# Optimization experiments

Hardware: AMD Instinct MI355X
Metric: run time of the kernel (lower is better)

The kernel has to match this reference:

```python
import jax, jax.numpy as jnp
import numpy as np

B, H, O, E, CMAP = 8192, 1024, 256, 16, 1000


def setup_inputs() -> dict:
    key = jax.random.key(0)
    k_x, k_w, k_b, k_num, k_c = jax.random.split(key, 5)
    x = jax.random.normal(k_x, (B, H), dtype=jnp.float32)
    num = jax.random.randint(k_num, (B,), 0, CMAP, dtype=jnp.int64)
    c = jax.random.randint(k_c, (CMAP,), 0, E, dtype=jnp.int64)
    # per-expert Linear params (torch default: uniform(-1/sqrt(H), 1/sqrt(H)))
    bound = 1.0 / np.sqrt(H)
    W = jax.random.uniform(k_w, (E, O, H), dtype=jnp.float32, minval=-bound, maxval=bound)
    b = jax.random.uniform(k_b, (E, O), dtype=jnp.float32, minval=-bound, maxval=bound)
    return {"x": x, "W": W, "b": b, "num": num, "c": c}


def reference(x, W, b, num, c):
    # expert id for each sample: layers[c[num[i]]]
    expert = c[num]  # [B]
    # compute all experts' linear outputs in one batched GEMM, then select.
    # logits: [B, E, O]
    logits = jnp.einsum('bh,eoh->beo', x, W) + b[None, :, :]
    sel = jnp.take_along_axis(logits, expert[:, None, None], axis=1)[:, 0, :]  # [B, O]
    return jax.nn.sigmoid(sel)
```

## Files before the change

kernel.cpp:

```cpp
#include <hip/hip_runtime.h>
#include <hip/hip_bf16.h>
#include <stdint.h>

#define B_N   8192
#define H_K   1024
#define O_N   256
#define E_N   16
#define RCAP  1024

#define TILE_M    64
#define TILE_N    128
#define BK        64
#define NITER     (H_K / BK)
#define MAX_TILES (RCAP / TILE_M)

#define WS_CURSOR   0
#define WS_ROWBUF   1024
#define WS_XSORT    131072
#define WS_WBF16    (WS_XSORT + 33554432 + 131072)

typedef __attribute__((ext_vector_type(8))) short  short8;
typedef __attribute__((ext_vector_type(4))) float  float4v;

__device__ __forceinline__ short f32_to_bf16(float f) {
    uint32_t u = __builtin_bit_cast(uint32_t, f);
    u += 0x7fffu + ((u >> 16) & 1u);
    return (short)(u >> 16);
}

__device__ __forceinline__ short8 cvt8(float4v v0, float4v v1) {
    short8 s;
    s[0] = f32_to_bf16(v0[0]); s[1] = f32_to_bf16(v0[1]);
    s[2] = f32_to_bf16(v0[2]); s[3] = f32_to_bf16(v0[3]);
    s[4] = f32_to_bf16(v1[0]); s[5] = f32_to_bf16(v1[1]);
    s[6] = f32_to_bf16(v1[2]); s[7] = f32_to_bf16(v1[3]);
    return s;
}

__device__ __forceinline__ float4v mfma16(short8 a, short8 b, float4v c) {
    return __builtin_amdgcn_mfma_f32_16x16x32_bf16(a, b, c, 0, 0, 0);
}

__device__ __forceinline__ void gl2lds16(const void* gsrc, void* ldst) {
    __builtin_amdgcn_global_load_lds(
        (const __attribute__((address_space(1))) uint32_t*)gsrc,
        (__attribute__((address_space(3))) uint32_t*)ldst, 16, 0, 0);
}

__global__ __launch_bounds__(256) void
k_prep(const float* __restrict__ W, const int* __restrict__ num, const int* __restrict__ c,
       int* __restrict__ cursor, int* __restrict__ rowbuf, short* __restrict__ Wb) {
    const int tid = threadIdx.x;
    const int bx  = blockIdx.x;

    if (bx < 32) {
        __shared__ int lcnt[E_N], lbase[E_N], lcnt2[E_N];
        if (tid < E_N) { lcnt[tid] = 0; lcnt2[tid] = 0; }
        __syncthreads();
        const int i = bx * 256 + tid;
        const int e = c[num[i]];
        atomicAdd(&lcnt[e], 1);
        __syncthreads();
        if (tid < E_N) lbase[tid] = atomicAdd(&cursor[tid], lcnt[tid]);
        __syncthreads();
        const int r = atomicAdd(&lcnt2[e], 1);
        const int p = lbase[e] + r;
        if (p < RCAP) rowbuf[e * RCAP + p] = i;
    }

    const int nchunk = E_N * O_N * H_K / 8;
    const int stride = gridDim.x * blockDim.x;
    for (int ch = bx * 256 + tid; ch < nchunk; ch += stride) {
        const float4v* src = (const float4v*)(W + (size_t)ch * 8);
        *(short8*)(Wb + (size_t)ch * 8) = cvt8(src[0], src[1]);
    }
}

__global__ __launch_bounds__(256) void
k_reorder(const float* __restrict__ x, const int* __restrict__ cursor,
          const int* __restrict__ rowbuf, short* __restrict__ xsrt) {
    const int e = blockIdx.x, t = blockIdx.y, tid = threadIdx.x;
    int count = cursor[e]; if (count > RCAP) count = RCAP;
    const int lim = (count + TILE_M - 1) & ~(TILE_M - 1);
    const int p0 = t * 32;
    if (p0 >= lim) return;

#pragma unroll
    for (int it = 0; it < 16; ++it) {
        const int idx = tid + it * 256;
        const int rl = idx >> 7, ch = idx & 127;
        const int p = p0 + rl;
        if (p >= lim) continue;
        short8 s;
        if (p < count) {
            const int grow = rowbuf[e * RCAP + p];
            const float4v* src = (const float4v*)(x + (size_t)grow * H_K + ch * 8);
            s = cvt8(src[0], src[1]);
        } else {
            s = (short8)(short)0;
        }
        *(short8*)(xsrt + ((size_t)(e * RCAP + p)) * H_K + ch * 8) = s;
    }
}

__global__ __launch_bounds__(256) void
k_gemm(const short* __restrict__ xs_g, const short* __restrict__ Wb,
       const float* __restrict__ bias, const int* __restrict__ cursor,
       const int* __restrict__ rowbuf, float* __restrict__ out) {
    const int e = blockIdx.x;
    int count = cursor[e]; if (count > RCAP) count = RCAP;
    const int m0 = blockIdx.y * TILE_M;
    if (m0 >= count) return;
    const int n0 = blockIdx.z * TILE_N;

    __shared__ short xs[2][TILE_M][BK];
    __shared__ short wsh[2][TILE_N][BK];
    __shared__ int   rows[TILE_M];

    const int tid = threadIdx.x;
    if (tid < TILE_M)
        rows[tid] = (m0 + tid < count) ? rowbuf[e * RCAP + m0 + tid] : -1;

    const int lane = tid & 63;
    const int wave = tid >> 6;
    const int wm = wave >> 1, wn = wave & 1;
    const int quad = lane >> 4, l16 = lane & 15;

    const int sub = lane >> 3;
    const int clx = (lane & 7) ^ sub;

    const short* xseg = xs_g + (size_t)(e * RCAP + m0) * H_K;
    const short* wseg = Wb + (size_t)(e * O_N + n0) * H_K;

    auto issue = [&](int buf, int k0) {
#pragma unroll
        for (int u = 0; u < 2; ++u) {
            const int q = wave * 2 + u;
            gl2lds16(xseg + (size_t)(q * 8 + sub) * H_K + k0 + clx * 8, &xs[buf][q * 8][0]);
        }
#pragma unroll
        for (int u = 0; u < 4; ++u) {
            const int q = wave * 4 + u;
            gl2lds16(wseg + (size_t)(q * 8 + sub) * H_K + k0 + clx * 8, &wsh[buf][q * 8][0]);
        }
    };

    float4v acc[2][4];
#pragma unroll
    for (int i = 0; i < 2; ++i)
#pragma unroll
        for (int j = 0; j < 4; ++j) acc[i][j] = (float4v)0.0f;

    issue(0, 0);

    for (int k = 0; k < NITER; ++k) {
        const int cur = k & 1;
        __syncthreads();
        if (k + 1 < NITER) issue(1 - cur, (k + 1) * BK);

#pragma unroll
        for (int ks = 0; ks < 2; ++ks) {
            const int cl = ks * 4 + quad;
            const int cp = (cl ^ (l16 & 7)) * 8;
            short8 a0 = *(const short8*)&xs[cur][wm * 32 + l16][cp];
            short8 a1 = *(const short8*)&xs[cur][wm * 32 + 16 + l16][cp];
            short8 b0 = *(const short8*)&wsh[cur][wn * 64 + l16][cp];
            short8 b1 = *(const short8*)&wsh[cur][wn * 64 + 16 + l16][cp];
            short8 b2 = *(const short8*)&wsh[cur][wn * 64 + 32 + l16][cp];
            short8 b3 = *(const short8*)&wsh[cur][wn * 64 + 48 + l16][cp];
            acc[0][0] = mfma16(a0, b0, acc[0][0]);
            acc[0][1] = mfma16(a0, b1, acc[0][1]);
            acc[0][2] = mfma16(a0, b2, acc[0][2]);
            acc[0][3] = mfma16(a0, b3, acc[0][3]);
            acc[1][0] = mfma16(a1, b0, acc[1][0]);
            acc[1][1] = mfma16(a1, b1, acc[1][1]);
            acc[1][2] = mfma16(a1, b2, acc[1][2]);
            acc[1][3] = mfma16(a1, b3, acc[1][3]);
        }
    }

#pragma unroll
    for (int jn = 0; jn < 4; ++jn) {
        const int colg = n0 + wn * 64 + jn * 16 + l16;
        const float bv = bias[e * O_N + colg];
#pragma unroll
        for (int jm = 0; jm < 2; ++jm) {
            const int rl = wm * 32 + jm * 16 + quad * 4;
#pragma unroll
            for (int reg = 0; reg < 4; ++reg) {
                const int rid = rows[rl + reg];
                if (rid >= 0) {
                    const float v = acc[jm][jn][reg] + bv;
                    out[(size_t)rid * O_N + colg] = 1.0f / (1.0f + __expf(-v));
                }
            }
        }
    }
}

extern "C" void kernel_launch(void* const* d_in, const int* in_sizes, int n_in,
                              void* d_out, int out_size, void* d_ws, size_t ws_size,
                              hipStream_t stream) {
    const float* x   = (const float*)d_in[0];
    const float* W   = (const float*)d_in[1];
    const float* b   = (const float*)d_in[2];
    const int*   num = (const int*)d_in[3];
    const int*   c   = (const int*)d_in[4];
    float* out = (float*)d_out;

    char*  ws     = (char*)d_ws;
    int*   cursor = (int*)(ws + WS_CURSOR);
    int*   rowbuf = (int*)(ws + WS_ROWBUF);
    short* xsrt   = (short*)(ws + WS_XSORT);
    short* Wb     = (short*)(ws + WS_WBF16);

    hipMemsetAsync(cursor, 0, E_N * sizeof(int), stream);
    k_prep<<<256, 256, 0, stream>>>(W, num, c, cursor, rowbuf, Wb);

    dim3 gr(E_N, RCAP / 32);
    k_reorder<<<gr, 256, 0, stream>>>(x, cursor, rowbuf, xsrt);

    dim3 gg(E_N, MAX_TILES, O_N / TILE_N);
    k_gemm<<<gg, 256, 0, stream>>>(xsrt, Wb, b, cursor, rowbuf, out);
}
```

Before: 134.6 us.

## Fuse x gather and bf16 conversion into GEMM, drop reorder kernel

Removes the separate reorder kernel. The GEMM now reads the selected fp32 rows of x directly, converts them to bf16 in registers and stores them into a padded LDS tile. The x loads are software-pipelined one step ahead of the async W loads. Expert bucketing is rewritten as one block per expert using bitmasks and a wave-shuffle prefix scan, which removes the atomics and the cursor memset. The M tile shrinks from 64 to 32. This avoids writing and re-reading a sorted bf16 copy of x and saves one launch. In exchange, x is read in fp32 once per N tile and W is re-read more often from cache. The per-expert rowbuf write also loses its RCAP bound check.

```diff
diff --git a/kernel.cpp b/kernel.cpp
--- a/kernel.cpp
+++ b/kernel.cpp
@@ -8,16 +8,16 @@
 #define E_N   16
 #define RCAP  1024
 
-#define TILE_M    64
+#define TILE_M    32
 #define TILE_N    128
 #define BK        64
 #define NITER     (H_K / BK)
-#define MAX_TILES (RCAP / TILE_M)
+#define MTILES    (RCAP / TILE_M)
+#define LDS_LD    (BK + 8)
 
 #define WS_CURSOR   0
 #define WS_ROWBUF   1024
-#define WS_XSORT    131072
-#define WS_WBF16    (WS_XSORT + 33554432 + 131072)
+#define WS_WBF16    131072
 
 typedef __attribute__((ext_vector_type(8))) short  short8;
 typedef __attribute__((ext_vector_type(4))) float  float4v;
@@ -53,23 +53,35 @@
     const int tid = threadIdx.x;
     const int bx  = blockIdx.x;
 
-    if (bx < 32) {
-        __shared__ int lcnt[E_N], lbase[E_N], lcnt2[E_N];
-        if (tid < E_N) { lcnt[tid] = 0; lcnt2[tid] = 0; }
+    if (bx < E_N) {
+        unsigned mask = 0;
+#pragma unroll
+        for (int u = 0; u < 32; ++u) {
+            const int i = u * 256 + tid;
+            const int e = c[num[i]];
+            mask |= (unsigned)(e == bx) << u;
+        }
+        const int cnt = __popc(mask);
+        const int lane = tid & 63, wv = tid >> 6;
+        int incl = cnt;
+#pragma unroll
+        for (int d = 1; d < 64; d <<= 1) {
+            int v = __shfl_up(incl, d, 64);
+            if (lane >= d) incl += v;
+        }
+        __shared__ int wsum[4];
+        if (lane == 63) wsum[wv] = incl;
         __syncthreads();
-        const int i = bx * 256 + tid;
-        const int e = c[num[i]];
-        atomicAdd(&lcnt[e], 1);
-        __syncthreads();
-        if (tid < E_N) lbase[tid] = atomicAdd(&cursor[tid], lcnt[tid]);
-        __syncthreads();
-        const int r = atomicAdd(&lcnt2[e], 1);
-        const int p = lbase[e] + r;
-        if (p < RCAP) rowbuf[e * RCAP + p] = i;
+        int base = 0;
+        for (int w = 0; w < wv; ++w) base += wsum[w];
+        int pos = base + incl - cnt;
+        for (int u = 0; u < 32; ++u)
+            if ((mask >> u) & 1u) rowbuf[bx * RCAP + pos++] = u * 256 + tid;
+        if (tid == 255) cursor[bx] = base + incl;
     }
 
     const int nchunk = E_N * O_N * H_K / 8;
-    const int stride = gridDim.x * blockDim.x;
+    const int stride = 256 * 256;
     for (int ch = bx * 256 + tid; ch < nchunk; ch += stride) {
         const float4v* src = (const float4v*)(W + (size_t)ch * 8);
         *(short8*)(Wb + (size_t)ch * 8) = cvt8(src[0], src[1]);
@@ -77,34 +89,7 @@
 }
 
 __global__ __launch_bounds__(256) void
-k_reorder(const float* __restrict__ x, const int* __restrict__ cursor,
-          const int* __restrict__ rowbuf, short* __restrict__ xsrt) {
-    const int e = blockIdx.x, t = blockIdx.y, tid = threadIdx.x;
-    int count = cursor[e]; if (count > RCAP) count = RCAP;
-    const int lim = (count + TILE_M - 1) & ~(TILE_M - 1);
-    const int p0 = t * 32;
-    if (p0 >= lim) return;
-
-#pragma unroll
-    for (int it = 0; it < 16; ++it) {
-        const int idx = tid + it * 256;
-        const int rl = idx >> 7, ch = idx & 127;
-        const int p = p0 + rl;
-        if (p >= lim) continue;
-        short8 s;
-        if (p < count) {
-            const int grow = rowbuf[e * RCAP + p];
-            const float4v* src = (const float4v*)(x + (size_t)grow * H_K + ch * 8);
-            s = cvt8(src[0], src[1]);
-        } else {
-            s = (short8)(short)0;
-        }
-        *(short8*)(xsrt + ((size_t)(e * RCAP + p)) * H_K + ch * 8) = s;
-    }
-}
-
-__global__ __launch_bounds__(256) void
-k_gemm(const short* __restrict__ xs_g, const short* __restrict__ Wb,
+k_gemm(const float* __restrict__ x, const short* __restrict__ Wb,
        const float* __restrict__ bias, const int* __restrict__ cursor,
        const int* __restrict__ rowbuf, float* __restrict__ out) {
     const int e = blockIdx.x;
@@ -113,13 +98,18 @@
     if (m0 >= count) return;
     const int n0 = blockIdx.z * TILE_N;
 
-    __shared__ short xs[2][TILE_M][BK];
+    __shared__ short xs[2][TILE_M][LDS_LD];
     __shared__ short wsh[2][TILE_N][BK];
     __shared__ int   rows[TILE_M];
 
     const int tid = threadIdx.x;
     if (tid < TILE_M)
         rows[tid] = (m0 + tid < count) ? rowbuf[e * RCAP + m0 + tid] : -1;
+    __syncthreads();
+
+    const int r8   = tid >> 3;
+    const int scol = (tid & 7) * 8;
+    const int xrow = rows[r8];
 
     const int lane = tid & 63;
     const int wave = tid >> 6;
@@ -129,70 +119,72 @@
     const int sub = lane >> 3;
     const int clx = (lane & 7) ^ sub;
 
-    const short* xseg = xs_g + (size_t)(e * RCAP + m0) * H_K;
     const short* wseg = Wb + (size_t)(e * O_N + n0) * H_K;
 
-    auto issue = [&](int buf, int k0) {
-#pragma unroll
-        for (int u = 0; u < 2; ++u) {
-            const int q = wave * 2 + u;
-            gl2lds16(xseg + (size_t)(q * 8 + sub) * H_K + k0 + clx * 8, &xs[buf][q * 8][0]);
-        }
+    float4v xv0, xv1;
+    auto load_x = [&](int k0) {
+        if (xrow >= 0) {
+            const float4v* p = (const float4v*)(x + (size_t)xrow * H_K + k0 + scol);
+            xv0 = p[0]; xv1 = p[1];
+        } else { xv0 = (float4v)0.0f; xv1 = (float4v)0.0f; }
+    };
+    auto store_x = [&](int buf) {
+        *(short8*)&xs[buf][r8][scol] = cvt8(xv0, xv1);
+    };
+    auto issue_w = [&](int buf, int k0) {
 #pragma unroll
         for (int u = 0; u < 4; ++u) {
             const int q = wave * 4 + u;
-            gl2lds16(wseg + (size_t)(q * 8 + sub) * H_K + k0 + clx * 8, &wsh[buf][q * 8][0]);
+            gl2lds16(wseg + (size_t)(q * 8 + sub) * H_K + k0 + clx * 8,
+                     &wsh[buf][q * 8][0]);
         }
     };
 
-    float4v acc[2][4];
-#pragma unroll
-    for (int i = 0; i < 2; ++i)
-#pragma unroll
-        for (int j = 0; j < 4; ++j) acc[i][j] = (float4v)0.0f;
-
-    issue(0, 0);
+    float4v acc[4];
+#pragma unroll
+    for (int j = 0; j < 4; ++j) acc[j] = (float4v)0.0f;
+
+    load_x(0);
+    issue_w(0, 0);
+    store_x(0);
 
     for (int k = 0; k < NITER; ++k) {
         const int cur = k & 1;
         __syncthreads();
-        if (k + 1 < NITER) issue(1 - cur, (k + 1) * BK);
+        if (k + 1 < NITER) {
+            load_x((k + 1) * BK);
+            issue_w(1 - cur, (k + 1) * BK);
+        }
 
 #pragma unroll
         for (int ks = 0; ks < 2; ++ks) {
-            const int cl = ks * 4 + quad;
-            const int cp = (cl ^ (l16 & 7)) * 8;
-            short8 a0 = *(const short8*)&xs[cur][wm * 32 + l16][cp];
-            short8 a1 = *(const short8*)&xs[cur][wm * 32 + 16 + l16][cp];
-            short8 b0 = *(const short8*)&wsh[cur][wn * 64 + l16][cp];
-            short8 b1 = *(const short8*)&wsh[cur][wn * 64 + 16 + l16][cp];
-            short8 b2 = *(const short8*)&wsh[cur][wn * 64 + 32 + l16][cp];
-            short8 b3 = *(const short8*)&wsh[cur][wn * 64 + 48 + l16][cp];
-            acc[0][0] = mfma16(a0, b0, acc[0][0]);
-            acc[0][1] = mfma16(a0, b1, acc[0][1]);
-            acc[0][2] = mfma16(a0, b2, acc[0][2]);
-            acc[0][3] = mfma16(a0, b3, acc[0][3]);
-            acc[1][0] = mfma16(a1, b0, acc[1][0]);
-            acc[1][1] = mfma16(a1, b1, acc[1][1]);
-            acc[1][2] = mfma16(a1, b2, acc[1][2]);
-            acc[1][3] = mfma16(a1, b3, acc[1][3]);
-        }
-    }
-
-#pragma unroll
-    for (int jn = 0; jn < 4; ++jn) {
-        const int colg = n0 + wn * 64 + jn * 16 + l16;
+            const int kx = ks * 32 + quad * 8;
+            const int cw = (((ks * 4 + quad) ^ (l16 & 7))) * 8;
+            short8 a  = *(const short8*)&xs[cur][wm * 16 + l16][kx];
+            short8 b0 = *(const short8*)&wsh[cur][wn * 64 + l16][cw];
+            short8 b1 = *(const short8*)&wsh[cur][wn * 64 + 16 + l16][cw];
+            short8 b2 = *(const short8*)&wsh[cur][wn * 64 + 32 + l16][cw];
+            short8 b3 = *(const short8*)&wsh[cur][wn * 64 + 48 + l16][cw];
+            acc[0] = mfma16(a, b0, acc[0]);
+            acc[1] = mfma16(a, b1, acc[1]);
+            acc[2] = mfma16(a, b2, acc[2]);
+            acc[3] = mfma16(a, b3, acc[3]);
+        }
+
+        if (k + 1 < NITER) store_x(1 - cur);
+    }
+
+#pragma unroll
+    for (int j = 0; j < 4; ++j) {
+        const int colg = n0 + wn * 64 + j * 16 + l16;
         const float bv = bias[e * O_N + colg];
-#pragma unroll
-        for (int jm = 0; jm < 2; ++jm) {
-            const int rl = wm * 32 + jm * 16 + quad * 4;
-#pragma unroll
-            for (int reg = 0; reg < 4; ++reg) {
-                const int rid = rows[rl + reg];
-                if (rid >= 0) {
-                    const float v = acc[jm][jn][reg] + bv;
-                    out[(size_t)rid * O_N + colg] = 1.0f / (1.0f + __expf(-v));
-                }
+        const int rl = wm * 16 + quad * 4;
+#pragma unroll
+        for (int reg = 0; reg < 4; ++reg) {
+            const int rid = rows[rl + reg];
+            if (rid >= 0) {
+                const float v = acc[j][reg] + bv;
+                out[(size_t)rid * O_N + colg] = 1.0f / (1.0f + __expf(-v));
             }
         }
     }
@@ -211,15 +203,10 @@
     char*  ws     = (char*)d_ws;
     int*   cursor = (int*)(ws + WS_CURSOR);
     int*   rowbuf = (int*)(ws + WS_ROWBUF);
-    short* xsrt   = (short*)(ws + WS_XSORT);
     short* Wb     = (short*)(ws + WS_WBF16);
 
-    hipMemsetAsync(cursor, 0, E_N * sizeof(int), stream);
     k_prep<<<256, 256, 0, stream>>>(W, num, c, cursor, rowbuf, Wb);
 
-    dim3 gr(E_N, RCAP / 32);
-    k_reorder<<<gr, 256, 0, stream>>>(x, cursor, rowbuf, xsrt);
-
-    dim3 gg(E_N, MAX_TILES, O_N / TILE_N);
-    k_gemm<<<gg, 256, 0, stream>>>(xsrt, Wb, b, cursor, rowbuf, out);
-}
+    dim3 gg(E_N, MTILES, O_N / TILE_N);
+    k_gemm<<<gg, 256, 0, stream>>>(x, Wb, b, cursor, rowbuf, out);
+}
```

After: 115.9 us. 13.8% less time.
